# Kernel optimization log

Measured on AMD Instinct MI355X. Metric: run time of the kernel, lower is better.

## Reference

```python
import jax, jax.numpy as jnp
import numpy as np

B, N, DIN, D, H, L, DOUT = 32, 512, 256, 256, 8, 2, 256
DH = D // H
EPS = 1e-5
MAX_DEG, NUM_SPATIAL = 1000, 100


def _bn(x, g, b):
    # torch BatchNorm1d training-mode normalization (biased variance over dim 0)
    m = x.mean(0)
    v = x.var(0)
    return (x - m) * jax.lax.rsqrt(v + EPS) * g + b


def _ln(x, g, b):
    m = x.mean(-1, keepdims=True)
    v = x.var(-1, keepdims=True)
    return (x - m) * jax.lax.rsqrt(v + EPS) * g + b


def _leaky(x):
    return jnp.where(x >= 0, x, 0.01 * x)


def setup_inputs() -> dict:
    key = jax.random.key(0)
    ks = iter(jax.random.split(key, 40))
    nrm = lambda shape: jax.random.normal(next(ks), shape, jnp.float32) * 0.02
    inp = {
        "x": jax.random.normal(next(ks), (B * N, DIN), jnp.float32),
        "adj_fc": jax.random.randint(next(ks), (B, N, N), 0, 2, jnp.int32),
        "spd_dist": jax.random.randint(next(ks), (B, N, N), -1, NUM_SPATIAL, jnp.int32),
        # lin_first: Linear + BatchNorm1d + LeakyReLU
        "W_first": nrm((D, DIN)), "b_first": jnp.zeros((D,), jnp.float32),
        "bn1_g": jnp.ones((D,), jnp.float32), "bn1_b": jnp.zeros((D,), jnp.float32),
        # embeddings (spd_embedding has padding_idx=0 -> zero row)
        "deg_emb": nrm((MAX_DEG, D)),
        "spd_emb": nrm((NUM_SPATIAL, H)).at[0].set(0.0),
        # stacked TransformerEncoderLayer params [L, ...]
        "Wqkv": nrm((L, 3 * D, D)), "bqkv": jnp.zeros((L, 3 * D), jnp.float32),
        "Wo": nrm((L, D, D)), "bo": jnp.zeros((L, D), jnp.float32),
        "ln1_g": jnp.ones((L, D), jnp.float32), "ln1_b": jnp.zeros((L, D), jnp.float32),
        "W1": nrm((L, D, D)), "b1": jnp.zeros((L, D), jnp.float32),
        "W2": nrm((L, D, D)), "b2": jnp.zeros((L, D), jnp.float32),
        "ln2_g": jnp.ones((L, D), jnp.float32), "ln2_b": jnp.zeros((L, D), jnp.float32),
        # lin_in: Linear + BatchNorm1d + LeakyReLU
        "W_in": nrm((DOUT, D)), "b_in": jnp.zeros((DOUT,), jnp.float32),
        "bn2_g": jnp.ones((DOUT,), jnp.float32), "bn2_b": jnp.zeros((DOUT,), jnp.float32),
    }
    return inp


def _forward(x, adj_fc, spd_dist, W_first, b_first, bn1_g, bn1_b, deg_emb, spd_emb,
             Wqkv, bqkv, Wo, bo, ln1_g, ln1_b, W1, b1, W2, b2, ln2_g, ln2_b,
             W_in, b_in, bn2_g, bn2_b):
    h = _leaky(_bn(x @ W_first.T + b_first, bn1_g, bn1_b)).reshape(B, N, D)
    # degree bias: adj_fc.bool().sum(1) -> [B, N]
    deg = (adj_fc != 0).sum(1)
    h = h + deg_emb[deg]
    # SPD-based per-head additive attention bias
    neg = spd_dist < 0
    am = spd_emb[jnp.where(neg, 0, spd_dist)]            # [B, N, N, H]
    am = jnp.where(neg[..., None], -1.0, am)
    # torch.cat over dim 0 per head -> [H*B, N, N]; torch MHA then consumes it
    # row-major as (b*H + h); replicate that exact (buggy-but-faithful) layout
    bias = jnp.concatenate([am[..., i] for i in range(H)], axis=0).reshape(B, H, N, N)
    scale = 1.0 / np.sqrt(DH).astype(np.float32)
    for l in range(L):
        qkv = h @ Wqkv[l].T + bqkv[l]                    # [B, N, 3D]
        q, k, v = jnp.split(qkv, 3, axis=-1)
        q = q.reshape(B, N, H, DH).transpose(0, 2, 1, 3)
        k = k.reshape(B, N, H, DH).transpose(0, 2, 1, 3)
        v = v.reshape(B, N, H, DH).transpose(0, 2, 1, 3)
        s = jnp.einsum('bhqd,bhkd->bhqk', q, k) * scale + bias
        p = jax.nn.softmax(s, axis=-1)
        o = jnp.einsum('bhqk,bhkd->bhqd', p, v).transpose(0, 2, 1, 3).reshape(B, N, D)
        h = _ln(h + o @ Wo[l].T + bo[l], ln1_g[l], ln1_b[l])  # post-norm
        f = jax.nn.relu(h @ W1[l].T + b1[l]) @ W2[l].T + b2[l]
        h = _ln(h + f, ln2_g[l], ln2_b[l])
    return _leaky(_bn(h.reshape(B * N, D) @ W_in.T + b_in, bn2_g, bn2_b))


def reference(x, adj_fc, spd_dist, W_first, b_first, bn1_g, bn1_b, deg_emb, spd_emb,
              Wqkv, bqkv, Wo, bo, ln1_g, ln1_b, W1, b1, W2, b2, ln2_g, ln2_b,
              W_in, b_in, bn2_g, bn2_b):
    return _forward(x, adj_fc, spd_dist, W_first, b_first, bn1_g, bn1_b, deg_emb,
                    spd_emb, Wqkv, bqkv, Wo, bo, ln1_g, ln1_b, W1, b1, W2, b2,
                    ln2_g, ln2_b, W_in, b_in, bn2_g, bn2_b)
```

## Files before the change

### kernel.cpp

```cpp
#include <hip/hip_runtime.h>
#include <hip/hip_bf16.h>
#include <math.h>

#define B_   32
#define N_   512
#define D_   256
#define H_   8
#define DH_  32
#define L_   2
#define ROWS (B_ * N_)
#define EPS_ 1e-5f

typedef __attribute__((ext_vector_type(8))) short bf16x8;
typedef __attribute__((ext_vector_type(4))) float f32x4;

__device__ __forceinline__ short f2bf(float f) {
    unsigned u = __builtin_bit_cast(unsigned, f);
    u += 0x7fffu + ((u >> 16) & 1u);
    return (short)(u >> 16);
}

__device__ __forceinline__ void gl_lds16(const short* g, short* l) {
    __builtin_amdgcn_global_load_lds(
        (const __attribute__((address_space(1))) unsigned int*)g,
        (__attribute__((address_space(3))) unsigned int*)l, 16, 0, 0);
}

__global__ __launch_bounds__(256) void cvt_all(const float* __restrict__ x,
                                               const float* __restrict__ wf,
                                               const float* __restrict__ wq,
                                               const float* __restrict__ wo,
                                               const float* __restrict__ w1,
                                               const float* __restrict__ w2,
                                               const float* __restrict__ wi,
                                               short* __restrict__ xb,
                                               short* __restrict__ wb)
{
    const int u = blockIdx.x * 256 + threadIdx.x;
    if (u >= 638976) return;
    const float* s; short* d; int off;
    if      (u < 524288) { s = x;  d = xb;          off = u; }
    else if (u < 532480) { s = wf; d = wb;          off = u - 524288; }
    else if (u < 581632) { s = wq; d = wb + 65536;  off = u - 532480; }
    else if (u < 598016) { s = wo; d = wb + 458752; off = u - 581632; }
    else if (u < 614400) { s = w1; d = wb + 589824; off = u - 598016; }
    else if (u < 630784) { s = w2; d = wb + 720896; off = u - 614400; }
    else                 { s = wi; d = wb + 851968; off = u - 630784; }
    const float4 a = ((const float4*)s)[off * 2];
    const float4 b = ((const float4*)s)[off * 2 + 1];
    bf16x8 o;
    o[0] = f2bf(a.x); o[1] = f2bf(a.y); o[2] = f2bf(a.z); o[3] = f2bf(a.w);
    o[4] = f2bf(b.x); o[5] = f2bf(b.y); o[6] = f2bf(b.z); o[7] = f2bf(b.w);
    *(bf16x8*)(d + (size_t)off * 8) = o;
}

template<int FLAGS>
__global__ __launch_bounds__(256) void gemm_bf16(const short* __restrict__ A,
                                                 const short* __restrict__ Bw,
                                                 const float* __restrict__ bias,
                                                 float* __restrict__ Cf,
                                                 short* __restrict__ Cb,
                                                 int M, int Nn, int K)
{
    __shared__ short Al[128 * 64];
    __shared__ short Bl[128 * 64];
    const int t = threadIdx.x, w = t >> 6, l = t & 63;
    const int lg = l >> 4, lr = l & 15;
    const int wm = w >> 1, wn = w & 1;
    const int m0 = blockIdx.x * 128, n0 = blockIdx.y * 128;
    const int srow = w * 32 + (l >> 3), sslot = l & 7;

    f32x4 acc[4][4] = {};

    for (int kb = 0; kb < K; kb += 64) {
        if (kb) __syncthreads();
        #pragma unroll
        for (int j = 0; j < 4; j++) {
            const int ra = srow + j * 8;
            const int sw = (sslot ^ (ra & 7)) << 3;
            gl_lds16(A  + (size_t)(m0 + ra) * K + kb + sw, &Al[(w * 32 + j * 8) * 64]);
            gl_lds16(Bw + (size_t)(n0 + ra) * K + kb + sw, &Bl[(w * 32 + j * 8) * 64]);
        }
        __syncthreads();
        #pragma unroll
        for (int ks = 0; ks < 2; ks++) {
            bf16x8 af[4], bfr[4];
            #pragma unroll
            for (int i = 0; i < 4; i++) {
                const int ar = wm * 64 + i * 16 + lr;
                af[i]  = *(const bf16x8*)&Al[ar * 64 + (((lg + ks * 4) ^ (ar & 7)) << 3)];
                const int br = wn * 64 + i * 16 + lr;
                bfr[i] = *(const bf16x8*)&Bl[br * 64 + (((lg + ks * 4) ^ (br & 7)) << 3)];
            }
            #pragma unroll
            for (int mi = 0; mi < 4; mi++)
                #pragma unroll
                for (int ni = 0; ni < 4; ni++)
                    acc[mi][ni] = __builtin_amdgcn_mfma_f32_16x16x32_bf16(af[mi], bfr[ni],
                                                                          acc[mi][ni], 0, 0, 0);
        }
    }

    #pragma unroll
    for (int ni = 0; ni < 4; ni++) {
        const int n = n0 + wn * 64 + ni * 16 + lr;
        const float bv = bias[n];
        const float qs = ((FLAGS & 8) && n < 256) ? 0.17677669529663687f : 1.0f;
        #pragma unroll
        for (int mi = 0; mi < 4; mi++) {
            #pragma unroll
            for (int r = 0; r < 4; r++) {
                const int m = m0 + wm * 64 + mi * 16 + 4 * lg + r;
                float v = (acc[mi][ni][r] + bv) * qs;
                if (FLAGS & 4) v = fmaxf(v, 0.f);
                if (FLAGS & 1) Cf[(size_t)m * Nn + n] = v;
                if (FLAGS & 2) Cb[(size_t)m * Nn + n] = f2bf(v);
            }
        }
    }
}

__global__ __launch_bounds__(256) void bn_partial(const float* __restrict__ Y,
                                                  float* __restrict__ part)
{
    const int t = threadIdx.x, blk = blockIdx.x;
    float s = 0.f, sq = 0.f;
    const float* p = Y + (size_t)blk * 256 * 256 + t;
    for (int r = 0; r < 256; r++) {
        float v = p[(size_t)r * 256];
        s += v; sq += v * v;
    }
    part[blk * 512 + t]       = s;
    part[blk * 512 + 256 + t] = sq;
}

__global__ __launch_bounds__(256) void bn_finalize(const float* __restrict__ part,
                                                   const float* __restrict__ g,
                                                   const float* __restrict__ b,
                                                   float* __restrict__ sc)
{
    const int t = threadIdx.x;
    float s = 0.f, sq = 0.f;
    for (int i = 0; i < 64; i++) { s += part[i * 512 + t]; sq += part[i * 512 + 256 + t]; }
    const float mean = s * (1.f / (float)ROWS);
    const float var  = sq * (1.f / (float)ROWS) - mean * mean;
    const float k    = g[t] * rsqrtf(var + EPS_);
    sc[t]       = k;
    sc[256 + t] = b[t] - mean * k;
}

__global__ __launch_bounds__(256) void bn_apply_leaky(const float* __restrict__ Y,
                                                      const float* __restrict__ sc,
                                                      float* __restrict__ O)
{
    const int idx = blockIdx.x * 256 + threadIdx.x;
    const int c4  = (idx & 63) * 4;
    const float4 v  = *(const float4*)&Y[(size_t)idx * 4];
    const float4 k  = *(const float4*)&sc[c4];
    const float4 sh = *(const float4*)&sc[256 + c4];
    float4 o;
    o.x = fmaf(v.x, k.x, sh.x); o.x = o.x >= 0.f ? o.x : 0.01f * o.x;
    o.y = fmaf(v.y, k.y, sh.y); o.y = o.y >= 0.f ? o.y : 0.01f * o.y;
    o.z = fmaf(v.z, k.z, sh.z); o.z = o.z >= 0.f ? o.z : 0.01f * o.z;
    o.w = fmaf(v.w, k.w, sh.w); o.w = o.w >= 0.f ? o.w : 0.01f * o.w;
    *(float4*)&O[(size_t)idx * 4] = o;
}

__global__ __launch_bounds__(256) void deg_kernel(const int* __restrict__ adj,
                                                  int* __restrict__ deg)
{
    const int b = blockIdx.x;
    const int j = blockIdx.y * 256 + threadIdx.x;
    const int* p = adj + (size_t)b * N_ * N_ + j;
    int c = 0;
    for (int i = 0; i < N_; i++) c += (p[(size_t)i * N_] != 0);
    deg[b * N_ + j] = c;
}

__global__ __launch_bounds__(256) void deg_add2(const int* __restrict__ deg,
                                                const float* __restrict__ emb,
                                                float* __restrict__ h,
                                                short* __restrict__ hb)
{
    const int idx = blockIdx.x * 256 + threadIdx.x;
    const int row = idx >> 6;
    const int c4  = (idx & 63) * 4;
    const int d   = deg[row];
    const float4 e = *(const float4*)&emb[(size_t)d * 256 + c4];
    float4 v = *(float4*)&h[(size_t)idx * 4];
    v.x += e.x; v.y += e.y; v.z += e.z; v.w += e.w;
    *(float4*)&h[(size_t)idx * 4] = v;
    short4 s; s.x = f2bf(v.x); s.y = f2bf(v.y); s.z = f2bf(v.z); s.w = f2bf(v.w);
    *(short4*)&hb[(size_t)idx * 4] = s;
}

__global__ __launch_bounds__(256) void add_ln2(float* __restrict__ h,
                                               short* __restrict__ hb,
                                               const float* __restrict__ p,
                                               const float* __restrict__ g,
                                               const float* __restrict__ be)
{
    const int wv = threadIdx.x >> 6, ln = threadIdx.x & 63;
    const size_t row  = (size_t)blockIdx.x * 4 + wv;
    const size_t base = row * 256 + ln * 4;
    const float4 a = *(const float4*)&h[base];
    const float4 q = *(const float4*)&p[base];
    const float v0 = a.x + q.x, v1 = a.y + q.y, v2 = a.z + q.z, v3 = a.w + q.w;
    float s  = v0 + v1 + v2 + v3;
    float sq = v0 * v0 + v1 * v1 + v2 * v2 + v3 * v3;
    #pragma unroll
    for (int m = 1; m < 64; m <<= 1) {
        s  += __shfl_xor(s,  m, 64);
        sq += __shfl_xor(sq, m, 64);
    }
    const float mean = s * (1.f / 256.f);
    const float var  = sq * (1.f / 256.f) - mean * mean;
    const float r    = rsqrtf(var + EPS_);
    const float4 gg = *(const float4*)&g[ln * 4];
    const float4 bb = *(const float4*)&be[ln * 4];
    float4 o;
    o.x = (v0 - mean) * r * gg.x + bb.x;
    o.y = (v1 - mean) * r * gg.y + bb.y;
    o.z = (v2 - mean) * r * gg.z + bb.z;
    o.w = (v3 - mean) * r * gg.w + bb.w;
    *(float4*)&h[base] = o;
    short4 sb; sb.x = f2bf(o.x); sb.y = f2bf(o.y); sb.z = f2bf(o.z); sb.w = f2bf(o.w);
    *(short4*)&hb[base] = sb;
}

#define KST 40
#define VST 136
#define PST 136

__global__ __launch_bounds__(256) void attn_mfma(const short* __restrict__ qkv,
                                                 const int* __restrict__ spd,
                                                 const float* __restrict__ semb,
                                                 short* __restrict__ out)
{
    __shared__ short Kl[128 * KST];
    __shared__ short Vl[32 * VST];
    __shared__ short Pl[4][16 * PST];
    __shared__ float sembL[128];

    const int t  = threadIdx.x, w = t >> 6, l = t & 63;
    const int lg = l >> 4, lr = l & 15;

    const int s   = ((blockIdx.x & 7) << 7) + (blockIdx.x >> 3);
    const int bs  = s >> 5, ie = (s >> 2) & 7, qb = s & 3;
    const int b   = (ie * 32 + bs) >> 3, hd = (ie * 32 + bs) & 7;
    const int q0  = qb * 128 + w * 32;

    if (t < 100) sembL[t] = semb[t * 8 + ie];

    bf16x8 qf[2];
    #pragma unroll
    for (int qt = 0; qt < 2; qt++)
        qf[qt] = *(const bf16x8*)&qkv[((size_t)b * N_ + q0 + qt * 16 + lr) * 768 + hd * 32 + lg * 8];

    f32x4 oacc[2][2] = {};
    float mrun[2] = {-INFINITY, -INFINITY}, srun[2] = {0.f, 0.f};

    const int sr = t >> 1, shf = (t & 1) << 4;

    for (int k0 = 0; k0 < N_; k0 += 128) {
        if (k0) __syncthreads();
        {
            const short* kg = qkv + ((size_t)b * N_ + k0 + sr) * 768 + 256 + hd * 32 + shf;
            *(bf16x8*)&Kl[sr * KST + shf]     = *(const bf16x8*)kg;
            *(bf16x8*)&Kl[sr * KST + shf + 8] = *(const bf16x8*)(kg + 8);
            const bf16x8 v0 = *(const bf16x8*)(kg + 256);
            const bf16x8 v1 = *(const bf16x8*)(kg + 264);
            #pragma unroll
            for (int i = 0; i < 8; i++) {
                Vl[(shf + i)     * VST + sr] = v0[i];
                Vl[(shf + 8 + i) * VST + sr] = v1[i];
            }
        }
        __syncthreads();

        bf16x8 kfr[8];
        #pragma unroll
        for (int ct = 0; ct < 8; ct++)
            kfr[ct] = *(const bf16x8*)&Kl[(ct * 16 + lr) * KST + lg * 8];
        bf16x8 vfr[4][2];
        #pragma unroll
        for (int kt = 0; kt < 4; kt++)
            #pragma unroll
            for (int c2 = 0; c2 < 2; c2++)
                vfr[kt][c2] = *(const bf16x8*)&Vl[(c2 * 16 + lr) * VST + kt * 32 + lg * 8];

        #pragma unroll
        for (int qt = 0; qt < 2; qt++) {
            const int4* sp4 = (const int4*)(spd + ((size_t)bs * N_ + q0 + qt * 16 + lr) * N_ + k0);
            f32x4 sA[8];
            #pragma unroll
            for (int ct = 0; ct < 8; ct++) {
                const int4 sv = sp4[ct * 4 + lg];
                f32x4 c;
                c[0] = (sv.x < 0) ? -1.0f : sembL[sv.x];
                c[1] = (sv.y < 0) ? -1.0f : sembL[sv.y];
                c[2] = (sv.z < 0) ? -1.0f : sembL[sv.z];
                c[3] = (sv.w < 0) ? -1.0f : sembL[sv.w];
                sA[ct] = c;
            }
            #pragma unroll
            for (int ct = 0; ct < 8; ct++)
                sA[ct] = __builtin_amdgcn_mfma_f32_16x16x32_bf16(kfr[ct], qf[qt], sA[ct], 0, 0, 0);

            float m = sA[0][0];
            #pragma unroll
            for (int ct = 0; ct < 8; ct++)
                #pragma unroll
                for (int r = 0; r < 4; r++) m = fmaxf(m, sA[ct][r]);
            m = fmaxf(m, __shfl_xor(m, 16, 64));
            m = fmaxf(m, __shfl_xor(m, 32, 64));
            const float mnew  = fmaxf(mrun[qt], m);
            const float alpha = __expf(mrun[qt] - mnew);
            mrun[qt] = mnew;

            float ps = 0.f;
            #pragma unroll
            for (int ct = 0; ct < 8; ct++) {
                float p0 = __expf(sA[ct][0] - mnew);
                float p1 = __expf(sA[ct][1] - mnew);
                float p2 = __expf(sA[ct][2] - mnew);
                float p3 = __expf(sA[ct][3] - mnew);
                ps += (p0 + p1) + (p2 + p3);
                short4 pk; pk.x = f2bf(p0); pk.y = f2bf(p1); pk.z = f2bf(p2); pk.w = f2bf(p3);
                *(short4*)&Pl[w][lr * PST + ct * 16 + 4 * lg] = pk;
            }
            ps += __shfl_xor(ps, 16, 64);
            ps += __shfl_xor(ps, 32, 64);
            srun[qt] = srun[qt] * alpha + ps;
            oacc[qt][0] *= alpha;
            oacc[qt][1] *= alpha;

            #pragma unroll
            for (int kt = 0; kt < 4; kt++) {
                const bf16x8 pa = *(const bf16x8*)&Pl[w][lr * PST + kt * 32 + lg * 8];
                #pragma unroll
                for (int c2 = 0; c2 < 2; c2++)
                    oacc[qt][c2] = __builtin_amdgcn_mfma_f32_16x16x32_bf16(vfr[kt][c2], pa,
                                                                           oacc[qt][c2], 0, 0, 0);
            }
        }
    }

    #pragma unroll
    for (int qt = 0; qt < 2; qt++) {
        const float inv = 1.f / srun[qt];
        #pragma unroll
        for (int c2 = 0; c2 < 2; c2++) {
            short4 s4;
            s4.x = f2bf(oacc[qt][c2][0] * inv);
            s4.y = f2bf(oacc[qt][c2][1] * inv);
            s4.z = f2bf(oacc[qt][c2][2] * inv);
            s4.w = f2bf(oacc[qt][c2][3] * inv);
            *(short4*)&out[((size_t)b * N_ + q0 + qt * 16 + lr) * 256 + hd * 32 + c2 * 16 + 4 * lg] = s4;
        }
    }
}

extern "C" void kernel_launch(void* const* d_in, const int* in_sizes, int n_in,
                              void* d_out, int out_size, void* d_ws, size_t ws_size,
                              hipStream_t stream)
{
    const float* x    = (const float*)d_in[0];
    const int*   adj  = (const int*)  d_in[1];
    const int*   spd  = (const int*)  d_in[2];
    const float* Wf   = (const float*)d_in[3];
    const float* bf   = (const float*)d_in[4];
    const float* bn1g = (const float*)d_in[5];
    const float* bn1b = (const float*)d_in[6];
    const float* degE = (const float*)d_in[7];
    const float* semb = (const float*)d_in[8];
    const float* Wqkv = (const float*)d_in[9];
    const float* bqkv = (const float*)d_in[10];
    const float* Wo   = (const float*)d_in[11];
    const float* bo   = (const float*)d_in[12];
    const float* ln1g = (const float*)d_in[13];
    const float* ln1b = (const float*)d_in[14];
    const float* W1   = (const float*)d_in[15];
    const float* b1   = (const float*)d_in[16];
    const float* W2   = (const float*)d_in[17];
    const float* b2   = (const float*)d_in[18];
    const float* ln2g = (const float*)d_in[19];
    const float* ln2b = (const float*)d_in[20];
    const float* Win  = (const float*)d_in[21];
    const float* bin  = (const float*)d_in[22];
    const float* bn2g = (const float*)d_in[23];
    const float* bn2b = (const float*)d_in[24];

    char* p = (char*)d_ws;
    float* h    = (float*)p;  p += (size_t)ROWS * 256 * 4;
    float* t3   = (float*)p;  p += (size_t)ROWS * 256 * 4;
    char*  shr  = p;          p += (size_t)ROWS * 768 * 2;
    float* t1   = (float*)shr;
    short* qkvb = (short*)shr;
    short* hb   = (short*)p;  p += (size_t)ROWS * 256 * 2;
    short* t2b  = (short*)p;  p += (size_t)ROWS * 256 * 2;
    short* xb   = (short*)p;  p += (size_t)ROWS * 256 * 2;
    short* wb   = (short*)p;  p += (size_t)917504 * 2;
    int*   deg  = (int*)p;    p += (size_t)ROWS * 4;
    float* bnp  = (float*)p;  p += 64 * 512 * 4;
    float* bnf  = (float*)p;

    const short* wfb = wb;
    const short* wqb = wb + 65536;
    const short* wob = wb + 458752;
    const short* w1b = wb + 589824;
    const short* w2b = wb + 720896;
    const short* wib = wb + 851968;

    const dim3 blk(256);
    const dim3 g256(128, 2);
    const dim3 g768(128, 6);

    cvt_all<<<2496, blk, 0, stream>>>(x, Wf, Wqkv, Wo, W1, W2, Win, xb, wb);

    gemm_bf16<1><<<g256, blk, 0, stream>>>(xb, wfb, bf, t1, nullptr, ROWS, 256, 256);
    bn_partial <<<64, blk, 0, stream>>>(t1, bnp);
    bn_finalize<<<1,  blk, 0, stream>>>(bnp, bn1g, bn1b, bnf);
    bn_apply_leaky<<<ROWS * 256 / 4 / 256, blk, 0, stream>>>(t1, bnf, h);

    deg_kernel<<<dim3(B_, N_ / 256), blk, 0, stream>>>(adj, deg);
    deg_add2  <<<ROWS * 256 / 4 / 256, blk, 0, stream>>>(deg, degE, h, hb);

    for (int l = 0; l < L_; l++) {
        gemm_bf16<2 | 8><<<g768, blk, 0, stream>>>(hb, wqb + (size_t)l * 768 * 256,
                                                   bqkv + l * 768, nullptr, qkvb, ROWS, 768, 256);
        attn_mfma<<<1024, blk, 0, stream>>>(qkvb, spd, semb, t2b);
        gemm_bf16<1><<<g256, blk, 0, stream>>>(t2b, wob + (size_t)l * 256 * 256,
                                               bo + l * 256, t3, nullptr, ROWS, 256, 256);
        add_ln2<<<ROWS / 4, blk, 0, stream>>>(h, hb, t3, ln1g + l * 256, ln1b + l * 256);
        gemm_bf16<2 | 4><<<g256, blk, 0, stream>>>(hb, w1b + (size_t)l * 256 * 256,
                                                   b1 + l * 256, nullptr, t2b, ROWS, 256, 256);
        gemm_bf16<1><<<g256, blk, 0, stream>>>(t2b, w2b + (size_t)l * 256 * 256,
                                               b2 + l * 256, t3, nullptr, ROWS, 256, 256);
        add_ln2<<<ROWS / 4, blk, 0, stream>>>(h, hb, t3, ln2g + l * 256, ln2b + l * 256);
    }

    gemm_bf16<1><<<g256, blk, 0, stream>>>(hb, wib, bin, t1, nullptr, ROWS, 256, 256);
    bn_partial <<<64, blk, 0, stream>>>(t1, bnp);
    bn_finalize<<<1,  blk, 0, stream>>>(bnp, bn2g, bn2b, bnf);
    bn_apply_leaky<<<ROWS * 256 / 4 / 256, blk, 0, stream>>>(t1, bnf, (float*)d_out);
}
```

Baseline: 510.9 us.

## Double-buffer GEMM and attention K/V loads, fuse BN with degree add, parallelize degree

The GEMM now uses two LDS buffers so the global-to-LDS load of the next K tile is issued before the current tile's MFMAs. Attention prefetches the next K/V tile into registers during compute, and the V layout is padded to change bank mapping. BN apply/leaky and the degree-embedding add are merged into one elementwise kernel, and the degree count is split across more blocks with an LDS reduction. BN partials are transposed so the finalize step can read them as vectors. In exchange, LDS use and register pressure go up, which may reduce occupancy.

```diff
diff --git a/kernel.cpp b/kernel.cpp
--- a/kernel.cpp
+++ b/kernel.cpp
@@ -54,6 +54,19 @@
     *(bf16x8*)(d + (size_t)off * 8) = o;
 }
 
+#define GSTAGE(buf, kb)                                                        \
+    {                                                                          \
+        _Pragma("unroll")                                                      \
+        for (int j = 0; j < 4; j++) {                                          \
+            const int ra = srow + j * 8;                                       \
+            const int sw = (sslot ^ (ra & 7)) << 3;                            \
+            gl_lds16(A  + (size_t)(m0 + ra) * K + (kb) + sw,                   \
+                     &Al[buf][(w * 32 + j * 8) * 64]);                         \
+            gl_lds16(Bw + (size_t)(n0 + ra) * K + (kb) + sw,                   \
+                     &Bl[buf][(w * 32 + j * 8) * 64]);                         \
+        }                                                                      \
+    }
+
 template<int FLAGS>
 __global__ __launch_bounds__(256) void gemm_bf16(const short* __restrict__ A,
                                                  const short* __restrict__ Bw,
@@ -62,8 +75,8 @@
                                                  short* __restrict__ Cb,
                                                  int M, int Nn, int K)
 {
-    __shared__ short Al[128 * 64];
-    __shared__ short Bl[128 * 64];
+    __shared__ short Al[2][128 * 64];
+    __shared__ short Bl[2][128 * 64];
     const int t = threadIdx.x, w = t >> 6, l = t & 63;
     const int lg = l >> 4, lr = l & 15;
     const int wm = w >> 1, wn = w & 1;
@@ -72,25 +85,20 @@
 
     f32x4 acc[4][4] = {};
 
-    for (int kb = 0; kb < K; kb += 64) {
-        if (kb) __syncthreads();
-        #pragma unroll
-        for (int j = 0; j < 4; j++) {
-            const int ra = srow + j * 8;
-            const int sw = (sslot ^ (ra & 7)) << 3;
-            gl_lds16(A  + (size_t)(m0 + ra) * K + kb + sw, &Al[(w * 32 + j * 8) * 64]);
-            gl_lds16(Bw + (size_t)(n0 + ra) * K + kb + sw, &Bl[(w * 32 + j * 8) * 64]);
-        }
-        __syncthreads();
+    GSTAGE(0, 0);
+    __syncthreads();
+    int cur = 0;
+    for (int kb = 64; kb < K + 64; kb += 64) {
+        if (kb < K) GSTAGE(cur ^ 1, kb);
         #pragma unroll
         for (int ks = 0; ks < 2; ks++) {
             bf16x8 af[4], bfr[4];
             #pragma unroll
             for (int i = 0; i < 4; i++) {
                 const int ar = wm * 64 + i * 16 + lr;
-                af[i]  = *(const bf16x8*)&Al[ar * 64 + (((lg + ks * 4) ^ (ar & 7)) << 3)];
+                af[i]  = *(const bf16x8*)&Al[cur][ar * 64 + (((lg + ks * 4) ^ (ar & 7)) << 3)];
                 const int br = wn * 64 + i * 16 + lr;
-                bfr[i] = *(const bf16x8*)&Bl[br * 64 + (((lg + ks * 4) ^ (br & 7)) << 3)];
+                bfr[i] = *(const bf16x8*)&Bl[cur][br * 64 + (((lg + ks * 4) ^ (br & 7)) << 3)];
             }
             #pragma unroll
             for (int mi = 0; mi < 4; mi++)
@@ -99,6 +107,8 @@
                     acc[mi][ni] = __builtin_amdgcn_mfma_f32_16x16x32_bf16(af[mi], bfr[ni],
                                                                           acc[mi][ni], 0, 0, 0);
         }
+        __syncthreads();
+        cur ^= 1;
     }
 
     #pragma unroll
@@ -130,8 +140,8 @@
         float v = p[(size_t)r * 256];
         s += v; sq += v * v;
     }
-    part[blk * 512 + t]       = s;
-    part[blk * 512 + 256 + t] = sq;
+    part[t * 64 + blk]         = s;
+    part[16384 + t * 64 + blk] = sq;
 }
 
 __global__ __launch_bounds__(256) void bn_finalize(const float* __restrict__ part,
@@ -141,7 +151,13 @@
 {
     const int t = threadIdx.x;
     float s = 0.f, sq = 0.f;
-    for (int i = 0; i < 64; i++) { s += part[i * 512 + t]; sq += part[i * 512 + 256 + t]; }
+    #pragma unroll
+    for (int i = 0; i < 16; i++) {
+        const float4 a = *(const float4*)&part[t * 64 + i * 4];
+        const float4 q = *(const float4*)&part[16384 + t * 64 + i * 4];
+        s  += (a.x + a.y) + (a.z + a.w);
+        sq += (q.x + q.y) + (q.z + q.w);
+    }
     const float mean = s * (1.f / (float)ROWS);
     const float var  = sq * (1.f / (float)ROWS) - mean * mean;
     const float k    = g[t] * rsqrtf(var + EPS_);
@@ -166,32 +182,46 @@
     *(float4*)&O[(size_t)idx * 4] = o;
 }
 
-__global__ __launch_bounds__(256) void deg_kernel(const int* __restrict__ adj,
-                                                  int* __restrict__ deg)
-{
-    const int b = blockIdx.x;
-    const int j = blockIdx.y * 256 + threadIdx.x;
-    const int* p = adj + (size_t)b * N_ * N_ + j;
-    int c = 0;
-    for (int i = 0; i < N_; i++) c += (p[(size_t)i * N_] != 0);
-    deg[b * N_ + j] = c;
-}
-
-__global__ __launch_bounds__(256) void deg_add2(const int* __restrict__ deg,
-                                                const float* __restrict__ emb,
-                                                float* __restrict__ h,
-                                                short* __restrict__ hb)
+__global__ __launch_bounds__(256) void bn_deg(const float* __restrict__ Y,
+                                              const float* __restrict__ sc,
+                                              const int* __restrict__ deg,
+                                              const float* __restrict__ emb,
+                                              float* __restrict__ h,
+                                              short* __restrict__ hb)
 {
     const int idx = blockIdx.x * 256 + threadIdx.x;
     const int row = idx >> 6;
     const int c4  = (idx & 63) * 4;
-    const int d   = deg[row];
+    const float4 v  = *(const float4*)&Y[(size_t)idx * 4];
+    const float4 k  = *(const float4*)&sc[c4];
+    const float4 sh = *(const float4*)&sc[256 + c4];
+    const int d = deg[row];
     const float4 e = *(const float4*)&emb[(size_t)d * 256 + c4];
-    float4 v = *(float4*)&h[(size_t)idx * 4];
-    v.x += e.x; v.y += e.y; v.z += e.z; v.w += e.w;
-    *(float4*)&h[(size_t)idx * 4] = v;
-    short4 s; s.x = f2bf(v.x); s.y = f2bf(v.y); s.z = f2bf(v.z); s.w = f2bf(v.w);
-    *(short4*)&hb[(size_t)idx * 4] = s;
+    float4 o;
+    o.x = fmaf(v.x, k.x, sh.x); o.x = (o.x >= 0.f ? o.x : 0.01f * o.x) + e.x;
+    o.y = fmaf(v.y, k.y, sh.y); o.y = (o.y >= 0.f ? o.y : 0.01f * o.y) + e.y;
+    o.z = fmaf(v.z, k.z, sh.z); o.z = (o.z >= 0.f ? o.z : 0.01f * o.z) + e.z;
+    o.w = fmaf(v.w, k.w, sh.w); o.w = (o.w >= 0.f ? o.w : 0.01f * o.w) + e.w;
+    *(float4*)&h[(size_t)idx * 4] = o;
+    short4 s4; s4.x = f2bf(o.x); s4.y = f2bf(o.y); s4.z = f2bf(o.z); s4.w = f2bf(o.w);
+    *(short4*)&hb[(size_t)idx * 4] = s4;
+}
+
+__global__ __launch_bounds__(256) void deg_kernel(const int* __restrict__ adj,
+                                                  int* __restrict__ deg)
+{
+    __shared__ int sm[4][64];
+    const int b = blockIdx.x, j0 = blockIdx.y * 64;
+    const int tg = threadIdx.x >> 6, lane = threadIdx.x & 63;
+    const int* p = adj + (size_t)b * N_ * N_ + j0 + lane;
+    int c = 0;
+    #pragma unroll 4
+    for (int i = tg; i < N_; i += 4) c += (p[(size_t)i * N_] != 0);
+    sm[tg][lane] = c;
+    __syncthreads();
+    if (threadIdx.x < 64)
+        deg[b * N_ + j0 + threadIdx.x] =
+            sm[0][threadIdx.x] + sm[1][threadIdx.x] + sm[2][threadIdx.x] + sm[3][threadIdx.x];
 }
 
 __global__ __launch_bounds__(256) void add_ln2(float* __restrict__ h,
@@ -238,7 +268,7 @@
                                                  short* __restrict__ out)
 {
     __shared__ short Kl[128 * KST];
-    __shared__ short Vl[32 * VST];
+    __shared__ short Vl[32 * VST + 64];
     __shared__ short Pl[4][16 * PST];
     __shared__ float sembL[128];
 
@@ -261,23 +291,24 @@
     float mrun[2] = {-INFINITY, -INFINITY}, srun[2] = {0.f, 0.f};
 
     const int sr = t >> 1, shf = (t & 1) << 4;
-
-    for (int k0 = 0; k0 < N_; k0 += 128) {
-        if (k0) __syncthreads();
-        {
-            const short* kg = qkv + ((size_t)b * N_ + k0 + sr) * 768 + 256 + hd * 32 + shf;
-            *(bf16x8*)&Kl[sr * KST + shf]     = *(const bf16x8*)kg;
-            *(bf16x8*)&Kl[sr * KST + shf + 8] = *(const bf16x8*)(kg + 8);
-            const bf16x8 v0 = *(const bf16x8*)(kg + 256);
-            const bf16x8 v1 = *(const bf16x8*)(kg + 264);
-            #pragma unroll
-            for (int i = 0; i < 8; i++) {
-                Vl[(shf + i)     * VST + sr] = v0[i];
-                Vl[(shf + 8 + i) * VST + sr] = v1[i];
-            }
-        }
-        __syncthreads();
-
+    const int vofs = (t & 1) * 32;
+    const short* kgBase = qkv + ((size_t)b * N_ + sr) * 768 + 256 + hd * 32 + shf;
+
+    bf16x8 nk0 = *(const bf16x8*)(kgBase);
+    bf16x8 nk1 = *(const bf16x8*)(kgBase + 8);
+    bf16x8 nv0 = *(const bf16x8*)(kgBase + 256);
+    bf16x8 nv1 = *(const bf16x8*)(kgBase + 264);
+    *(bf16x8*)&Kl[sr * KST + shf]     = nk0;
+    *(bf16x8*)&Kl[sr * KST + shf + 8] = nk1;
+    #pragma unroll
+    for (int i = 0; i < 8; i++) {
+        Vl[(shf + i)     * VST + vofs + sr] = nv0[i];
+        Vl[(shf + 8 + i) * VST + vofs + sr] = nv1[i];
+    }
+    __syncthreads();
+
+    for (int ti = 0; ti < 4; ti++) {
+        const int k0 = ti * 128;
         bf16x8 kfr[8];
         #pragma unroll
         for (int ct = 0; ct < 8; ct++)
@@ -287,7 +318,13 @@
         for (int kt = 0; kt < 4; kt++)
             #pragma unroll
             for (int c2 = 0; c2 < 2; c2++)
-                vfr[kt][c2] = *(const bf16x8*)&Vl[(c2 * 16 + lr) * VST + kt * 32 + lg * 8];
+                vfr[kt][c2] = *(const bf16x8*)&Vl[(c2 * 16 + lr) * VST + c2 * 32 + kt * 32 + lg * 8];
+
+        const short* kgN = kgBase + (size_t)(((ti + 1) & 3) * 128) * 768;
+        nk0 = *(const bf16x8*)(kgN);
+        nk1 = *(const bf16x8*)(kgN + 8);
+        nv0 = *(const bf16x8*)(kgN + 256);
+        nv1 = *(const bf16x8*)(kgN + 264);
 
         #pragma unroll
         for (int qt = 0; qt < 2; qt++) {
@@ -343,6 +380,18 @@
                     oacc[qt][c2] = __builtin_amdgcn_mfma_f32_16x16x32_bf16(vfr[kt][c2], pa,
                                                                            oacc[qt][c2], 0, 0, 0);
             }
+        }
+
+        if (ti < 3) {
+            __syncthreads();
+            *(bf16x8*)&Kl[sr * KST + shf]     = nk0;
+            *(bf16x8*)&Kl[sr * KST + shf + 8] = nk1;
+            #pragma unroll
+            for (int i = 0; i < 8; i++) {
+                Vl[(shf + i)     * VST + vofs + sr] = nv0[i];
+                Vl[(shf + 8 + i) * VST + vofs + sr] = nv1[i];
+            }
+            __syncthreads();
         }
     }
 
@@ -417,14 +466,12 @@
     const dim3 g768(128, 6);
 
     cvt_all<<<2496, blk, 0, stream>>>(x, Wf, Wqkv, Wo, W1, W2, Win, xb, wb);
+    deg_kernel<<<dim3(B_, 8), blk, 0, stream>>>(adj, deg);
 
     gemm_bf16<1><<<g256, blk, 0, stream>>>(xb, wfb, bf, t1, nullptr, ROWS, 256, 256);
     bn_partial <<<64, blk, 0, stream>>>(t1, bnp);
     bn_finalize<<<1,  blk, 0, stream>>>(bnp, bn1g, bn1b, bnf);
-    bn_apply_leaky<<<ROWS * 256 / 4 / 256, blk, 0, stream>>>(t1, bnf, h);
-
-    deg_kernel<<<dim3(B_, N_ / 256), blk, 0, stream>>>(adj, deg);
-    deg_add2  <<<ROWS * 256 / 4 / 256, blk, 0, stream>>>(deg, degE, h, hb);
+    bn_deg<<<ROWS * 256 / 4 / 256, blk, 0, stream>>>(t1, bnf, deg, degE, h, hb);
 
     for (int l = 0; l < L_; l++) {
         gemm_bf16<2 | 8><<<g768, blk, 0, stream>>>(hb, wqb + (size_t)l * 768 * 256,
```

Measured after the change: 493.5 us. 1.04x faster.
